# Kernel optimization log

Measured on AMD Instinct MI355X. Metric: run time of the kernel, lower is better.

## Reference

```python
import jax, jax.numpy as jnp
import numpy as np

N = 50000
E = 800000
IN = 128
H = 128
C = 64
BN_EPS = 1e-5


def gcn_conv(x, W, b, src, dst, n_nodes):
    # GCNConv: add self-loops, symmetric normalization D^-1/2 (A+I) D^-1/2, linear, bias
    deg = jax.ops.segment_sum(jnp.ones_like(dst, dtype=x.dtype), dst, num_segments=n_nodes)
    dinv = jnp.where(deg > 0, jax.lax.rsqrt(deg), jnp.zeros_like(deg))
    norm = dinv[src] * dinv[dst]                      # [E+N]
    h = x @ W                                         # [N, out]
    agg = jax.ops.segment_sum(norm[:, None] * h[src], dst, num_segments=n_nodes)
    return agg + b


def batch_norm_eval(x, gamma, beta, mean, var):
    return gamma * (x - mean) * jax.lax.rsqrt(var + BN_EPS) + beta


def setup_inputs() -> dict:
    key = jax.random.key(0)
    ks = jax.random.split(key, 16)
    inp = {
        "x": jax.random.normal(ks[0], (N, IN), dtype=jnp.float32),
        "edge_index": jax.random.randint(ks[1], (2, E), 0, N, dtype=jnp.int64),
        "W1": jax.random.normal(ks[2], (IN, H), dtype=jnp.float32) / np.sqrt(IN),
        "b1": jnp.zeros((H,), dtype=jnp.float32),
        "g1": jnp.ones((H,), dtype=jnp.float32),
        "be1": jnp.zeros((H,), dtype=jnp.float32),
        "m1": jax.random.normal(ks[3], (H,), dtype=jnp.float32) * 0.1,
        "v1": jax.random.uniform(ks[4], (H,), dtype=jnp.float32, minval=0.5, maxval=1.5),
        "W2": jax.random.normal(ks[5], (H, H), dtype=jnp.float32) / np.sqrt(H),
        "b2": jnp.zeros((H,), dtype=jnp.float32),
        "g2": jnp.ones((H,), dtype=jnp.float32),
        "be2": jnp.zeros((H,), dtype=jnp.float32),
        "m2": jax.random.normal(ks[6], (H,), dtype=jnp.float32) * 0.1,
        "v2": jax.random.uniform(ks[7], (H,), dtype=jnp.float32, minval=0.5, maxval=1.5),
        "W3": jax.random.normal(ks[8], (H, C), dtype=jnp.float32) / np.sqrt(H),
        "b3": jnp.zeros((C,), dtype=jnp.float32),
    }
    return inp


def reference(x, edge_index, W1, b1, g1, be1, m1, v1, W2, b2, g2, be2, m2, v2, W3, b3):
    # add self loops once (shared across layers, GCNConv cached=True)
    loop = jnp.arange(N, dtype=edge_index.dtype)
    src = jnp.concatenate([edge_index[0], loop])
    dst = jnp.concatenate([edge_index[1], loop])

    h = gcn_conv(x, W1, b1, src, dst, N)
    h = jax.nn.relu(batch_norm_eval(h, g1, be1, m1, v1))  # eval mode: dropout is identity
    h = gcn_conv(h, W2, b2, src, dst, N)
    h = jax.nn.relu(batch_norm_eval(h, g2, be2, m2, v2))
    out = gcn_conv(h, W3, b3, src, dst, N)
    return out
```

## Files before the change

### kernel.cpp

```cpp
#include <hip/hip_runtime.h>


#define SCAN_CHUNK 1024
#define NCHUNK 256
#define BSHIFT 8
#define BWID 256
#define ECAP 8192

typedef __attribute__((ext_vector_type(8))) short bf16x8;
typedef __attribute__((ext_vector_type(4))) float f32x4;

__device__ __forceinline__ float blo(unsigned p) { return __uint_as_float(p << 16); }
__device__ __forceinline__ float bhi(unsigned p) { return __uint_as_float(p & 0xffff0000u); }
__device__ __forceinline__ unsigned short f2b(float f) {
  unsigned u = __float_as_uint(f);
  unsigned r = (u + 0x7fffu + ((u >> 16) & 1u)) >> 16;
  return (unsigned short)r;
}

__global__ __launch_bounds__(256) void histprep_kernel(
    const int* __restrict__ ei32, const long long* __restrict__ ei64,
    int* __restrict__ counts, int E, int nbk,
    const float* __restrict__ W1, const float* __restrict__ W2,
    const float* __restrict__ W3,
    const float* __restrict__ b1, const float* __restrict__ g1,
    const float* __restrict__ be1, const float* __restrict__ m1,
    const float* __restrict__ v1,
    const float* __restrict__ b2, const float* __restrict__ g2,
    const float* __restrict__ be2, const float* __restrict__ m2,
    const float* __restrict__ v2,
    unsigned short* __restrict__ Wt1, unsigned short* __restrict__ Wt2,
    unsigned short* __restrict__ Wt3,
    float* __restrict__ sc1, float* __restrict__ sh1,
    float* __restrict__ sc2, float* __restrict__ sh2) {
  __shared__ int hist[BWID];
  __shared__ int s_is32;
  int k = blockIdx.x, t = threadIdx.x;
  if (k >= NCHUNK) {
    int i = (k - NCHUNK) * 256 + t;
    if (i < 16384) {
      int kk = i >> 7, c = i & 127;
      Wt1[c * 128 + kk] = f2b(W1[i]);
    } else if (i < 32768) {
      int j = i - 16384; int kk = j >> 7, c = j & 127;
      Wt2[c * 128 + kk] = f2b(W2[j]);
    } else if (i < 40960) {
      int j = i - 32768; int kk = j >> 6, c = j & 63;
      Wt3[c * 128 + kk] = f2b(W3[j]);
    } else if (i < 41088) {
      int c = i - 40960;
      float s = g1[c] * rsqrtf(v1[c] + 1e-5f);
      sc1[c] = s; sh1[c] = (b1[c] - m1[c]) * s + be1[c];
    } else if (i < 41216) {
      int c = i - 41088;
      float s = g2[c] * rsqrtf(v2[c] + 1e-5f);
      sc2[c] = s; sh2[c] = (b2[c] - m2[c]) * s + be2[c];
    }
    return;
  }
  hist[t] = 0;
  if (t == 0) s_is32 = 0;
  int CH = (E + NCHUNK - 1) / NCHUNK;
  int e0 = k * CH, e1 = min(e0 + CH, E);
  __syncthreads();
  if (t < 64 && e0 + t < E && ei32[2 * (e0 + t) + 1] != 0) atomicOr(&s_is32, 1);
  __syncthreads();
  int is32 = s_is32;
  for (int e = e0 + t; e < e1; e += 256) {
    int d = is32 ? ei32[E + e] : (int)ei64[E + e];
    atomicAdd(&hist[d >> BSHIFT], 1);
  }
  __syncthreads();
  if (t < nbk) counts[t * NCHUNK + k] = hist[t];
}

__global__ __launch_bounds__(256) void scan_partial_kernel(
    const int* __restrict__ src, int* __restrict__ bsum, int n) {
  __shared__ int wsum[4];
  int b = blockIdx.x, t = threadIdx.x;
  int lane = t & 63, wv = t >> 6;
  int i0 = b * SCAN_CHUNK + t * 4;
  int4 d4 = make_int4(0, 0, 0, 0);
  if (i0 + 3 < n) d4 = *(const int4*)&src[i0];
  else {
    if (i0 < n) d4.x = src[i0];
    if (i0 + 1 < n) d4.y = src[i0 + 1];
    if (i0 + 2 < n) d4.z = src[i0 + 2];
  }
  int s = d4.x + d4.y + d4.z + d4.w;
#pragma unroll
  for (int off = 32; off; off >>= 1) s += __shfl_xor(s, off);
  if (lane == 0) wsum[wv] = s;
  __syncthreads();
  if (t == 0) bsum[b] = wsum[0] + wsum[1] + wsum[2] + wsum[3];
}

__global__ __launch_bounds__(256) void scan_write_kernel(
    const int* __restrict__ src, const int* __restrict__ bsum,
    int* __restrict__ outp, int n, int nb) {
  __shared__ int woff[4];
  __shared__ int s_boff;
  int b = blockIdx.x, t = threadIdx.x;
  int lane = t & 63, wv = t >> 6;
  if (t < 64) {
    int v = (t < nb) ? bsum[t] : 0;
    int ic = v;
#pragma unroll
    for (int off = 1; off < 64; off <<= 1) {
      int u = __shfl_up(ic, off);
      if (t >= off) ic += u;
    }
    if (t == b) s_boff = ic - v;
    if (b == nb - 1 && t == 63) outp[n] = ic;
  }
  int i0 = b * SCAN_CHUNK + t * 4;
  int4 d4 = make_int4(0, 0, 0, 0);
  if (i0 + 3 < n) d4 = *(const int4*)&src[i0];
  else {
    if (i0 < n) d4.x = src[i0];
    if (i0 + 1 < n) d4.y = src[i0 + 1];
    if (i0 + 2 < n) d4.z = src[i0 + 2];
  }
  int tsum = d4.x + d4.y + d4.z + d4.w;
  int inc = tsum;
#pragma unroll
  for (int off = 1; off < 64; off <<= 1) {
    int u = __shfl_up(inc, off);
    if (lane >= off) inc += u;
  }
  if (lane == 63) woff[wv] = inc;
  __syncthreads();
  if (t == 0) {
    int r = 0;
#pragma unroll
    for (int w = 0; w < 4; ++w) { int sw = woff[w]; woff[w] = r; r += sw; }
  }
  __syncthreads();
  int p = inc - tsum + woff[wv] + s_boff;
  int dg[4] = {d4.x, d4.y, d4.z, d4.w};
#pragma unroll
  for (int j = 0; j < 4; ++j) {
    int i = i0 + j;
    if (i < n) outp[i] = p;
    p += dg[j];
  }
}

__global__ __launch_bounds__(256) void bin_scatter_kernel(
    const int* __restrict__ ei32, const long long* __restrict__ ei64,
    const int* __restrict__ offs, unsigned* __restrict__ pairs, int E, int nbk) {
  __shared__ int cur[BWID];
  __shared__ int s_is32;
  int k = blockIdx.x, t = threadIdx.x;
  if (t < nbk) cur[t] = offs[t * NCHUNK + k];
  if (t == 0) s_is32 = 0;
  int CH = (E + NCHUNK - 1) / NCHUNK;
  int e0 = k * CH, e1 = min(e0 + CH, E);
  __syncthreads();
  if (t < 64 && e0 + t < E && ei32[2 * (e0 + t) + 1] != 0) atomicOr(&s_is32, 1);
  __syncthreads();
  int is32 = s_is32;
  for (int e = e0 + t; e < e1; e += 256) {
    int s, d;
    if (is32) { s = ei32[e]; d = ei32[E + e]; }
    else      { s = (int)ei64[e]; d = (int)ei64[E + e]; }
    int pos = atomicAdd(&cur[d >> BSHIFT], 1);
    pairs[pos] = (unsigned)s | ((unsigned)(d & (BWID - 1)) << 20);
  }
}

__global__ __launch_bounds__(256) void bucket_merged_kernel(
    const unsigned* __restrict__ pairs, const int* __restrict__ offs,
    int* __restrict__ rowptr, float* __restrict__ dinv,
    int* __restrict__ col, int E, int n, int nbk) {
  __shared__ int deg[BWID];
  __shared__ int cur[BWID];
  __shared__ int woff[4];
  __shared__ int stage_s[ECAP];
  int b = blockIdx.x, t = threadIdx.x;
  int lane = t & 63, wv = t >> 6;
  deg[t] = 0;
  __syncthreads();
  int basep = offs[b * NCHUNK];
  int endp = (b + 1 < nbk) ? offs[(b + 1) * NCHUNK] : E;
  for (int i = basep + t; i < endp; i += 256)
    atomicAdd(&deg[pairs[i] >> 20], 1);
  __syncthreads();
  int dg = deg[t];
  int inc = dg;
#pragma unroll
  for (int off = 1; off < 64; off <<= 1) {
    int u = __shfl_up(inc, off);
    if (lane >= off) inc += u;
  }
  if (lane == 63) woff[wv] = inc;
  __syncthreads();
  if (t == 0) {
    int r = 0;
#pragma unroll
    for (int w = 0; w < 4; ++w) { int sw = woff[w]; woff[w] = r; r += sw; }
  }
  __syncthreads();
  int exc = inc - dg + woff[wv];
  int idx = b * BWID + t;
  if (idx < n) {
    rowptr[idx] = basep + exc;
    dinv[idx] = rsqrtf((float)(dg + 1));
  }
  cur[t] = exc;
  __syncthreads();
  for (int i = basep + t; i < endp; i += 256) {
    unsigned p = pairs[i];
    int s = (int)(p & 0xFFFFFu);
    int dl = (int)(p >> 20);
    int pos = atomicAdd(&cur[dl], 1);
    if (pos < ECAP) stage_s[pos] = s;
    else col[basep + pos] = s;
  }
  __syncthreads();
  int nE = endp - basep;
  int lim = min(nE, ECAP);
  for (int i = t; i < lim; i += 256) col[basep + i] = stage_s[i];
  if (b == 0 && t == 0) rowptr[n] = E;
}

template <int HOUT, int ABF16>
__global__ __launch_bounds__(256) void mgemm_kernel(
    const void* __restrict__ Ain, const unsigned short* __restrict__ Wt,
    unsigned short* __restrict__ Y, int n) {
  constexpr int NT = HOUT;
  __shared__ unsigned char AsB[64 * 256];
  __shared__ unsigned char BsB[NT * 256];
  int t = threadIdx.x;
  int row0 = blockIdx.x * 64;

  if constexpr (ABF16) {
    const unsigned short* A = (const unsigned short*)Ain;
#pragma unroll
    for (int jj = 0; jj < 4; ++jj) {
      int f = t + 256 * jj; int r = f >> 4, kq = f & 15;
      uint4 v = make_uint4(0, 0, 0, 0);
      if (row0 + r < n) v = *(const uint4*)&A[(size_t)(row0 + r) * 128 + kq * 8];
      *(uint4*)&AsB[r * 256 + ((kq * 16) ^ ((r & 15) << 4))] = v;
    }
  } else {
    const float* A = (const float*)Ain;
#pragma unroll
    for (int jj = 0; jj < 8; ++jj) {
      int f = t + 256 * jj; int r = f >> 5, kq = f & 31;
      float4 v = make_float4(0.f, 0.f, 0.f, 0.f);
      if (row0 + r < n) v = *(const float4*)&A[(size_t)(row0 + r) * 128 + kq * 4];
      unsigned two0 = (unsigned)f2b(v.x) | ((unsigned)f2b(v.y) << 16);
      unsigned two1 = (unsigned)f2b(v.z) | ((unsigned)f2b(v.w) << 16);
      uint2 o = make_uint2(two0, two1);
      *(uint2*)&AsB[r * 256 + ((kq * 8) ^ ((r & 15) << 4))] = o;
    }
  }
#pragma unroll
  for (int jj = 0; jj < NT / 16; ++jj) {
    int f = t + 256 * jj; int c = f >> 4, kq = f & 15;
    uint4 v = *(const uint4*)&Wt[(size_t)c * 128 + kq * 8];
    *(uint4*)&BsB[c * 256 + ((kq * 16) ^ ((c & 15) << 4))] = v;
  }
  __syncthreads();

  int l = t & 63, wid = t >> 6;
  constexpr int WC = NT / 2;
  constexpr int NI = WC / 16;
  int wr = (wid >> 1) * 32, wc = (wid & 1) * WC;
  int lr = l & 15, lk = (l >> 4) * 16;

  f32x4 acc[2][NI] = {};
#pragma unroll
  for (int ks = 0; ks < 4; ++ks) {
    bf16x8 a[2], b[NI];
#pragma unroll
    for (int mi = 0; mi < 2; ++mi) {
      int r = wr + mi * 16 + lr;
      a[mi] = *(const bf16x8*)&AsB[r * 256 + ((ks * 64 + lk) ^ ((r & 15) << 4))];
    }
#pragma unroll
    for (int ni = 0; ni < NI; ++ni) {
      int c = wc + ni * 16 + lr;
      b[ni] = *(const bf16x8*)&BsB[c * 256 + ((ks * 64 + lk) ^ ((c & 15) << 4))];
    }
#pragma unroll
    for (int mi = 0; mi < 2; ++mi)
#pragma unroll
      for (int ni = 0; ni < NI; ++ni)
        acc[mi][ni] = __builtin_amdgcn_mfma_f32_16x16x32_bf16(a[mi], b[ni],
                                                              acc[mi][ni], 0, 0, 0);
  }

#pragma unroll
  for (int mi = 0; mi < 2; ++mi) {
#pragma unroll
    for (int reg = 0; reg < 4; ++reg) {
      int gr = row0 + wr + mi * 16 + (l >> 4) * 4 + reg;
      if (gr < n) {
#pragma unroll
        for (int ni = 0; ni < NI; ++ni) {
          int gc = wc + ni * 16 + lr;
          Y[(size_t)gr * HOUT + gc] = f2b(acc[mi][ni][reg]);
        }
      }
    }
  }
}

template <int HOUT, bool BN, bool OUTBF>
__global__ __launch_bounds__(256) void agg_kernel(
    const unsigned short* __restrict__ h, const int* __restrict__ rowptr,
    const int* __restrict__ col, const float* __restrict__ dinv,
    const float* __restrict__ sc, const float* __restrict__ sh,
    void* __restrict__ out, int n_nodes) {
  int n = (blockIdx.x * blockDim.x + threadIdx.x) >> 6;
  if (n >= n_nodes) return;
  int lane = threadIdx.x & 63;
  const uint2* hu2 = (const uint2*)h;
  constexpr int RW2 = HOUT / 4;
  constexpr int NPH = (HOUT == 128) ? 2 : 4;
  constexpr int GL = 64 / NPH;
  int phase = lane / GL;
  int sub = lane & (GL - 1);

  float dn = dinv[n];
  int beg = rowptr[n], end = rowptr[n + 1];
  float a0 = 0.f, a1 = 0.f, a2 = 0.f, a3 = 0.f;
  if (phase == 0) {
    uint2 sp = hu2[(size_t)n * RW2 + sub];
    float sw = dn * dn;
    a0 = sw * blo(sp.x); a1 = sw * bhi(sp.x);
    a2 = sw * blo(sp.y); a3 = sw * bhi(sp.y);
  }

  int j = beg + phase;
  for (; j + 3 * NPH < end; j += 4 * NPH) {
    int s0 = col[j],           s1 = col[j + NPH];
    int s2 = col[j + 2 * NPH], s3 = col[j + 3 * NPH];
    uint2 h0 = hu2[(size_t)s0 * RW2 + sub];
    uint2 h1 = hu2[(size_t)s1 * RW2 + sub];
    uint2 h2 = hu2[(size_t)s2 * RW2 + sub];
    uint2 h3 = hu2[(size_t)s3 * RW2 + sub];
    float w0 = dn * dinv[s0], w1 = dn * dinv[s1];
    float w2 = dn * dinv[s2], w3 = dn * dinv[s3];
    a0 = fmaf(w0, blo(h0.x), a0); a1 = fmaf(w0, bhi(h0.x), a1);
    a2 = fmaf(w0, blo(h0.y), a2); a3 = fmaf(w0, bhi(h0.y), a3);
    a0 = fmaf(w1, blo(h1.x), a0); a1 = fmaf(w1, bhi(h1.x), a1);
    a2 = fmaf(w1, blo(h1.y), a2); a3 = fmaf(w1, bhi(h1.y), a3);
    a0 = fmaf(w2, blo(h2.x), a0); a1 = fmaf(w2, bhi(h2.x), a1);
    a2 = fmaf(w2, blo(h2.y), a2); a3 = fmaf(w2, bhi(h2.y), a3);
    a0 = fmaf(w3, blo(h3.x), a0); a1 = fmaf(w3, bhi(h3.x), a1);
    a2 = fmaf(w3, blo(h3.y), a2); a3 = fmaf(w3, bhi(h3.y), a3);
  }
  for (; j < end; j += NPH) {
    int s = col[j];
    uint2 hv = hu2[(size_t)s * RW2 + sub];
    float w = dn * dinv[s];
    a0 = fmaf(w, blo(hv.x), a0); a1 = fmaf(w, bhi(hv.x), a1);
    a2 = fmaf(w, blo(hv.y), a2); a3 = fmaf(w, bhi(hv.y), a3);
  }

  a0 += __shfl_xor(a0, 32); a1 += __shfl_xor(a1, 32);
  a2 += __shfl_xor(a2, 32); a3 += __shfl_xor(a3, 32);
  if constexpr (NPH == 4) {
    a0 += __shfl_xor(a0, 16); a1 += __shfl_xor(a1, 16);
    a2 += __shfl_xor(a2, 16); a3 += __shfl_xor(a3, 16);
  }
  if (phase != 0) return;

  int c0 = sub * 4;
  float y0, y1, y2, y3;
  if constexpr (BN) {
    y0 = fmaxf(fmaf(a0, sc[c0], sh[c0]), 0.f);
    y1 = fmaxf(fmaf(a1, sc[c0 + 1], sh[c0 + 1]), 0.f);
    y2 = fmaxf(fmaf(a2, sc[c0 + 2], sh[c0 + 2]), 0.f);
    y3 = fmaxf(fmaf(a3, sc[c0 + 3], sh[c0 + 3]), 0.f);
  } else {
    y0 = a0 + sh[c0]; y1 = a1 + sh[c0 + 1];
    y2 = a2 + sh[c0 + 2]; y3 = a3 + sh[c0 + 3];
  }
  if constexpr (OUTBF) {
    unsigned p0 = (unsigned)f2b(y0) | ((unsigned)f2b(y1) << 16);
    unsigned p1 = (unsigned)f2b(y2) | ((unsigned)f2b(y3) << 16);
    ((uint2*)out)[(size_t)n * RW2 + sub] = make_uint2(p0, p1);
  } else {
    float4 o; o.x = y0; o.y = y1; o.z = y2; o.w = y3;
    *(float4*)&((float*)out)[(size_t)n * HOUT + c0] = o;
  }
}

extern "C" void kernel_launch(void* const* d_in, const int* in_sizes, int n_in,
                              void* d_out, int out_size, void* d_ws, size_t ws_size,
                              hipStream_t stream) {
  const float* x = (const float*)d_in[0];
  const int* ei32 = (const int*)d_in[1];
  const long long* ei64 = (const long long*)d_in[1];
  const float* W1 = (const float*)d_in[2];
  const float* b1 = (const float*)d_in[3];
  const float* g1 = (const float*)d_in[4];
  const float* be1 = (const float*)d_in[5];
  const float* m1 = (const float*)d_in[6];
  const float* v1 = (const float*)d_in[7];
  const float* W2 = (const float*)d_in[8];
  const float* b2 = (const float*)d_in[9];
  const float* g2 = (const float*)d_in[10];
  const float* be2 = (const float*)d_in[11];
  const float* m2 = (const float*)d_in[12];
  const float* v2 = (const float*)d_in[13];
  const float* W3 = (const float*)d_in[14];
  const float* b3 = (const float*)d_in[15];

  const int N = in_sizes[0] / 128;
  const int E = in_sizes[1] / 2;
  const int NBK = (N + BWID - 1) / BWID;
  const int NC = NBK * NCHUNK;

  char* ws = (char*)d_ws;
  size_t off = 0;
  auto alloc = [&](size_t bytes) -> void* {
    void* p = ws + off;
    off = (off + bytes + 255) & ~(size_t)255;
    return p;
  };
  float* dinv = (float*)alloc((size_t)N * 4);
  int* rowptr = (int*)alloc((size_t)(N + 1) * 4);
  int* counts = (int*)alloc((size_t)(NC + 1) * 4);
  int* offs = (int*)alloc((size_t)(NC + 1) * 4);
  int* col = (int*)alloc((size_t)E * 4);
  unsigned* pairs = (unsigned*)alloc((size_t)E * 4);
  int* bsum = (int*)alloc(64 * 4);
  unsigned short* wt1 = (unsigned short*)alloc(128 * 128 * 2);
  unsigned short* wt2 = (unsigned short*)alloc(128 * 128 * 2);
  unsigned short* wt3 = (unsigned short*)alloc(128 * 64 * 2);
  float* sc1 = (float*)alloc(128 * 4);
  float* sh1 = (float*)alloc(128 * 4);
  float* sc2 = (float*)alloc(128 * 4);
  float* sh2 = (float*)alloc(128 * 4);
  unsigned short* hbuf = (unsigned short*)alloc((size_t)N * 128 * 2);
  unsigned short* ybuf = (unsigned short*)alloc((size_t)N * 128 * 2);
  (void)ws_size;

  histprep_kernel<<<NCHUNK + 161, 256, 0, stream>>>(
      ei32, ei64, counts, E, NBK,
      W1, W2, W3, b1, g1, be1, m1, v1, b2, g2, be2, m2, v2,
      wt1, wt2, wt3, sc1, sh1, sc2, sh2);
  int nbC = (NC + SCAN_CHUNK - 1) / SCAN_CHUNK;
  scan_partial_kernel<<<nbC, 256, 0, stream>>>(counts, bsum, NC);
  scan_write_kernel<<<nbC, 256, 0, stream>>>(counts, bsum, offs, NC, nbC);
  bin_scatter_kernel<<<NCHUNK, 256, 0, stream>>>(ei32, ei64, offs, pairs, E, NBK);
  bucket_merged_kernel<<<NBK, 256, 0, stream>>>(pairs, offs, rowptr, dinv,
                                                col, E, N, NBK);

  int gb = (N + 63) / 64;
  int ab = (N + 3) / 4;

  mgemm_kernel<128, 0><<<gb, 256, 0, stream>>>(x, wt1, hbuf, N);
  agg_kernel<128, true, true><<<ab, 256, 0, stream>>>(hbuf, rowptr, col, dinv,
                                                      sc1, sh1, ybuf, N);
  mgemm_kernel<128, 1><<<gb, 256, 0, stream>>>(ybuf, wt2, hbuf, N);
  agg_kernel<128, true, true><<<ab, 256, 0, stream>>>(hbuf, rowptr, col, dinv,
                                                      sc2, sh2, ybuf, N);
  mgemm_kernel<64, 1><<<gb, 256, 0, stream>>>(ybuf, wt3, hbuf, N);
  agg_kernel<64, false, false><<<ab, 256, 0, stream>>>(hbuf, rowptr, col, dinv,
                                                       nullptr, b3, d_out, N);
}
```

Measured before the change: 165.5 us.

## Fuse aggregation+BN+ReLU with the next layer's GEMM via shared-memory tile

Layers 1 and 2 now run as one kernel each: every block aggregates 64 node rows (one wave handles 16 rows in turn), applies BN and ReLU, writes the bf16 result into a swizzled LDS tile, and multiplies it by the next weight matrix with MFMA. This removes the round trip of the intermediate activation through global memory and two kernel launches. The cost is that each wave now processes rows one after another, which exposes gather latency, and there are fewer blocks than the old one-node-per-wave aggregation had. The final aggregation stays separate, specialised to 64 channels.

```diff
diff --git a/kernel.cpp b/kernel.cpp
--- a/kernel.cpp
+++ b/kernel.cpp
@@ -224,9 +224,9 @@
   if (b == 0 && t == 0) rowptr[n] = E;
 }
 
-template <int HOUT, int ABF16>
+template <int HOUT>
 __global__ __launch_bounds__(256) void mgemm_kernel(
-    const void* __restrict__ Ain, const unsigned short* __restrict__ Wt,
+    const float* __restrict__ A, const unsigned short* __restrict__ Wt,
     unsigned short* __restrict__ Y, int n) {
   constexpr int NT = HOUT;
   __shared__ unsigned char AsB[64 * 256];
@@ -234,27 +234,15 @@
   int t = threadIdx.x;
   int row0 = blockIdx.x * 64;
 
-  if constexpr (ABF16) {
-    const unsigned short* A = (const unsigned short*)Ain;
-#pragma unroll
-    for (int jj = 0; jj < 4; ++jj) {
-      int f = t + 256 * jj; int r = f >> 4, kq = f & 15;
-      uint4 v = make_uint4(0, 0, 0, 0);
-      if (row0 + r < n) v = *(const uint4*)&A[(size_t)(row0 + r) * 128 + kq * 8];
-      *(uint4*)&AsB[r * 256 + ((kq * 16) ^ ((r & 15) << 4))] = v;
-    }
-  } else {
-    const float* A = (const float*)Ain;
-#pragma unroll
-    for (int jj = 0; jj < 8; ++jj) {
-      int f = t + 256 * jj; int r = f >> 5, kq = f & 31;
-      float4 v = make_float4(0.f, 0.f, 0.f, 0.f);
-      if (row0 + r < n) v = *(const float4*)&A[(size_t)(row0 + r) * 128 + kq * 4];
-      unsigned two0 = (unsigned)f2b(v.x) | ((unsigned)f2b(v.y) << 16);
-      unsigned two1 = (unsigned)f2b(v.z) | ((unsigned)f2b(v.w) << 16);
-      uint2 o = make_uint2(two0, two1);
-      *(uint2*)&AsB[r * 256 + ((kq * 8) ^ ((r & 15) << 4))] = o;
-    }
+#pragma unroll
+  for (int jj = 0; jj < 8; ++jj) {
+    int f = t + 256 * jj; int r = f >> 5, kq = f & 31;
+    float4 v = make_float4(0.f, 0.f, 0.f, 0.f);
+    if (row0 + r < n) v = *(const float4*)&A[(size_t)(row0 + r) * 128 + kq * 4];
+    unsigned two0 = (unsigned)f2b(v.x) | ((unsigned)f2b(v.y) << 16);
+    unsigned two1 = (unsigned)f2b(v.z) | ((unsigned)f2b(v.w) << 16);
+    uint2 o = make_uint2(two0, two1);
+    *(uint2*)&AsB[r * 256 + ((kq * 8) ^ ((r & 15) << 4))] = o;
   }
 #pragma unroll
   for (int jj = 0; jj < NT / 16; ++jj) {
@@ -308,40 +296,158 @@
   }
 }
 
-template <int HOUT, bool BN, bool OUTBF>
-__global__ __launch_bounds__(256) void agg_kernel(
+template <int NTOUT>
+__global__ __launch_bounds__(256) void aggmm_kernel(
     const unsigned short* __restrict__ h, const int* __restrict__ rowptr,
     const int* __restrict__ col, const float* __restrict__ dinv,
     const float* __restrict__ sc, const float* __restrict__ sh,
-    void* __restrict__ out, int n_nodes) {
+    const unsigned short* __restrict__ Wt, unsigned short* __restrict__ Y,
+    int n_nodes) {
+  __shared__ unsigned char ytile[64 * 256];
+  __shared__ unsigned char BsB[NTOUT * 256];
+  const uint2* hu2 = (const uint2*)h;
+  int t = threadIdx.x;
+  int wv = t >> 6, lane = t & 63;
+  int row0 = blockIdx.x * 64;
+
+#pragma unroll
+  for (int jj = 0; jj < NTOUT / 16; ++jj) {
+    int f = t + 256 * jj; int c = f >> 4, kq = f & 15;
+    uint4 v = *(const uint4*)&Wt[(size_t)c * 128 + kq * 8];
+    *(uint4*)&BsB[c * 256 + ((kq * 16) ^ ((c & 15) << 4))] = v;
+  }
+
+  int phase = lane >> 5;
+  int sub = lane & 31;
+
+  for (int i = 0; i < 16; ++i) {
+    int r = wv * 16 + i;
+    int n = row0 + r;
+    float a0 = 0.f, a1 = 0.f, a2 = 0.f, a3 = 0.f;
+    if (n < n_nodes) {
+      float dn = dinv[n];
+      int beg = rowptr[n], end = rowptr[n + 1];
+      if (phase == 0) {
+        uint2 sp = hu2[(size_t)n * 32 + sub];
+        float sw = dn * dn;
+        a0 = sw * blo(sp.x); a1 = sw * bhi(sp.x);
+        a2 = sw * blo(sp.y); a3 = sw * bhi(sp.y);
+      }
+      int j = beg + phase;
+      for (; j + 6 < end; j += 8) {
+        int s0 = col[j], s1 = col[j + 2], s2 = col[j + 4], s3 = col[j + 6];
+        uint2 h0 = hu2[(size_t)s0 * 32 + sub];
+        uint2 h1 = hu2[(size_t)s1 * 32 + sub];
+        uint2 h2 = hu2[(size_t)s2 * 32 + sub];
+        uint2 h3 = hu2[(size_t)s3 * 32 + sub];
+        float w0 = dn * dinv[s0], w1 = dn * dinv[s1];
+        float w2 = dn * dinv[s2], w3 = dn * dinv[s3];
+        a0 = fmaf(w0, blo(h0.x), a0); a1 = fmaf(w0, bhi(h0.x), a1);
+        a2 = fmaf(w0, blo(h0.y), a2); a3 = fmaf(w0, bhi(h0.y), a3);
+        a0 = fmaf(w1, blo(h1.x), a0); a1 = fmaf(w1, bhi(h1.x), a1);
+        a2 = fmaf(w1, blo(h1.y), a2); a3 = fmaf(w1, bhi(h1.y), a3);
+        a0 = fmaf(w2, blo(h2.x), a0); a1 = fmaf(w2, bhi(h2.x), a1);
+        a2 = fmaf(w2, blo(h2.y), a2); a3 = fmaf(w2, bhi(h2.y), a3);
+        a0 = fmaf(w3, blo(h3.x), a0); a1 = fmaf(w3, bhi(h3.x), a1);
+        a2 = fmaf(w3, blo(h3.y), a2); a3 = fmaf(w3, bhi(h3.y), a3);
+      }
+      for (; j < end; j += 2) {
+        int s = col[j];
+        uint2 hv = hu2[(size_t)s * 32 + sub];
+        float w = dn * dinv[s];
+        a0 = fmaf(w, blo(hv.x), a0); a1 = fmaf(w, bhi(hv.x), a1);
+        a2 = fmaf(w, blo(hv.y), a2); a3 = fmaf(w, bhi(hv.y), a3);
+      }
+    }
+    a0 += __shfl_xor(a0, 32); a1 += __shfl_xor(a1, 32);
+    a2 += __shfl_xor(a2, 32); a3 += __shfl_xor(a3, 32);
+    if (phase == 0) {
+      unsigned p0 = 0, p1 = 0;
+      if (n < n_nodes) {
+        int c0 = sub * 4;
+        float y0 = fmaxf(fmaf(a0, sc[c0], sh[c0]), 0.f);
+        float y1 = fmaxf(fmaf(a1, sc[c0 + 1], sh[c0 + 1]), 0.f);
+        float y2 = fmaxf(fmaf(a2, sc[c0 + 2], sh[c0 + 2]), 0.f);
+        float y3 = fmaxf(fmaf(a3, sc[c0 + 3], sh[c0 + 3]), 0.f);
+        p0 = (unsigned)f2b(y0) | ((unsigned)f2b(y1) << 16);
+        p1 = (unsigned)f2b(y2) | ((unsigned)f2b(y3) << 16);
+      }
+      int byte = r * 256 + (((sub >> 1) * 16) ^ ((r & 15) << 4)) + ((sub & 1) * 8);
+      *(uint2*)&ytile[byte] = make_uint2(p0, p1);
+    }
+  }
+  __syncthreads();
+
+  constexpr int WC = NTOUT / 2;
+  constexpr int NI = WC / 16;
+  int wr = (wv >> 1) * 32, wc = (wv & 1) * WC;
+  int lr = lane & 15, lk = (lane >> 4) * 16;
+
+  f32x4 acc[2][NI] = {};
+#pragma unroll
+  for (int ks = 0; ks < 4; ++ks) {
+    bf16x8 a[2], b[NI];
+#pragma unroll
+    for (int mi = 0; mi < 2; ++mi) {
+      int r = wr + mi * 16 + lr;
+      a[mi] = *(const bf16x8*)&ytile[r * 256 + ((ks * 64 + lk) ^ ((r & 15) << 4))];
+    }
+#pragma unroll
+    for (int ni = 0; ni < NI; ++ni) {
+      int c = wc + ni * 16 + lr;
+      b[ni] = *(const bf16x8*)&BsB[c * 256 + ((ks * 64 + lk) ^ ((c & 15) << 4))];
+    }
+#pragma unroll
+    for (int mi = 0; mi < 2; ++mi)
+#pragma unroll
+      for (int ni = 0; ni < NI; ++ni)
+        acc[mi][ni] = __builtin_amdgcn_mfma_f32_16x16x32_bf16(a[mi], b[ni],
+                                                              acc[mi][ni], 0, 0, 0);
+  }
+
+#pragma unroll
+  for (int mi = 0; mi < 2; ++mi) {
+#pragma unroll
+    for (int reg = 0; reg < 4; ++reg) {
+      int gr = row0 + wr + mi * 16 + (lane >> 4) * 4 + reg;
+      if (gr < n_nodes) {
+#pragma unroll
+        for (int ni = 0; ni < NI; ++ni) {
+          int gc = wc + ni * 16 + lr;
+          Y[(size_t)gr * NTOUT + gc] = f2b(acc[mi][ni][reg]);
+        }
+      }
+    }
+  }
+}
+
+__global__ __launch_bounds__(256) void agg64_kernel(
+    const unsigned short* __restrict__ h, const int* __restrict__ rowptr,
+    const int* __restrict__ col, const float* __restrict__ dinv,
+    const float* __restrict__ bias, float* __restrict__ out, int n_nodes) {
   int n = (blockIdx.x * blockDim.x + threadIdx.x) >> 6;
   if (n >= n_nodes) return;
   int lane = threadIdx.x & 63;
   const uint2* hu2 = (const uint2*)h;
-  constexpr int RW2 = HOUT / 4;
-  constexpr int NPH = (HOUT == 128) ? 2 : 4;
-  constexpr int GL = 64 / NPH;
-  int phase = lane / GL;
-  int sub = lane & (GL - 1);
+  int phase = lane >> 4;
+  int sub = lane & 15;
 
   float dn = dinv[n];
   int beg = rowptr[n], end = rowptr[n + 1];
   float a0 = 0.f, a1 = 0.f, a2 = 0.f, a3 = 0.f;
   if (phase == 0) {
-    uint2 sp = hu2[(size_t)n * RW2 + sub];
+    uint2 sp = hu2[(size_t)n * 16 + sub];
     float sw = dn * dn;
     a0 = sw * blo(sp.x); a1 = sw * bhi(sp.x);
     a2 = sw * blo(sp.y); a3 = sw * bhi(sp.y);
   }
-
   int j = beg + phase;
-  for (; j + 3 * NPH < end; j += 4 * NPH) {
-    int s0 = col[j],           s1 = col[j + NPH];
-    int s2 = col[j + 2 * NPH], s3 = col[j + 3 * NPH];
-    uint2 h0 = hu2[(size_t)s0 * RW2 + sub];
-    uint2 h1 = hu2[(size_t)s1 * RW2 + sub];
-    uint2 h2 = hu2[(size_t)s2 * RW2 + sub];
-    uint2 h3 = hu2[(size_t)s3 * RW2 + sub];
+  for (; j + 12 < end; j += 16) {
+    int s0 = col[j], s1 = col[j + 4], s2 = col[j + 8], s3 = col[j + 12];
+    uint2 h0 = hu2[(size_t)s0 * 16 + sub];
+    uint2 h1 = hu2[(size_t)s1 * 16 + sub];
+    uint2 h2 = hu2[(size_t)s2 * 16 + sub];
+    uint2 h3 = hu2[(size_t)s3 * 16 + sub];
     float w0 = dn * dinv[s0], w1 = dn * dinv[s1];
     float w2 = dn * dinv[s2], w3 = dn * dinv[s3];
     a0 = fmaf(w0, blo(h0.x), a0); a1 = fmaf(w0, bhi(h0.x), a1);
@@ -353,41 +459,23 @@
     a0 = fmaf(w3, blo(h3.x), a0); a1 = fmaf(w3, bhi(h3.x), a1);
     a2 = fmaf(w3, blo(h3.y), a2); a3 = fmaf(w3, bhi(h3.y), a3);
   }
-  for (; j < end; j += NPH) {
+  for (; j < end; j += 4) {
     int s = col[j];
-    uint2 hv = hu2[(size_t)s * RW2 + sub];
+    uint2 hv = hu2[(size_t)s * 16 + sub];
     float w = dn * dinv[s];
     a0 = fmaf(w, blo(hv.x), a0); a1 = fmaf(w, bhi(hv.x), a1);
     a2 = fmaf(w, blo(hv.y), a2); a3 = fmaf(w, bhi(hv.y), a3);
   }
-
   a0 += __shfl_xor(a0, 32); a1 += __shfl_xor(a1, 32);
   a2 += __shfl_xor(a2, 32); a3 += __shfl_xor(a3, 32);
-  if constexpr (NPH == 4) {
-    a0 += __shfl_xor(a0, 16); a1 += __shfl_xor(a1, 16);
-    a2 += __shfl_xor(a2, 16); a3 += __shfl_xor(a3, 16);
-  }
+  a0 += __shfl_xor(a0, 16); a1 += __shfl_xor(a1, 16);
+  a2 += __shfl_xor(a2, 16); a3 += __shfl_xor(a3, 16);
   if (phase != 0) return;
-
   int c0 = sub * 4;
-  float y0, y1, y2, y3;
-  if constexpr (BN) {
-    y0 = fmaxf(fmaf(a0, sc[c0], sh[c0]), 0.f);
-    y1 = fmaxf(fmaf(a1, sc[c0 + 1], sh[c0 + 1]), 0.f);
-    y2 = fmaxf(fmaf(a2, sc[c0 + 2], sh[c0 + 2]), 0.f);
-    y3 = fmaxf(fmaf(a3, sc[c0 + 3], sh[c0 + 3]), 0.f);
-  } else {
-    y0 = a0 + sh[c0]; y1 = a1 + sh[c0 + 1];
-    y2 = a2 + sh[c0 + 2]; y3 = a3 + sh[c0 + 3];
-  }
-  if constexpr (OUTBF) {
-    unsigned p0 = (unsigned)f2b(y0) | ((unsigned)f2b(y1) << 16);
-    unsigned p1 = (unsigned)f2b(y2) | ((unsigned)f2b(y3) << 16);
-    ((uint2*)out)[(size_t)n * RW2 + sub] = make_uint2(p0, p1);
-  } else {
-    float4 o; o.x = y0; o.y = y1; o.z = y2; o.w = y3;
-    *(float4*)&((float*)out)[(size_t)n * HOUT + c0] = o;
-  }
+  float4 o;
+  o.x = a0 + bias[c0];     o.y = a1 + bias[c0 + 1];
+  o.z = a2 + bias[c0 + 2]; o.w = a3 + bias[c0 + 3];
+  *(float4*)&out[(size_t)n * 64 + c0] = o;
 }
 
 extern "C" void kernel_launch(void* const* d_in, const int* in_sizes, int n_in,
@@ -437,8 +525,9 @@
   float* sh1 = (float*)alloc(128 * 4);
   float* sc2 = (float*)alloc(128 * 4);
   float* sh2 = (float*)alloc(128 * 4);
-  unsigned short* hbuf = (unsigned short*)alloc((size_t)N * 128 * 2);
-  unsigned short* ybuf = (unsigned short*)alloc((size_t)N * 128 * 2);
+  unsigned short* hbufA = (unsigned short*)alloc((size_t)N * 128 * 2);
+  unsigned short* hbufB = (unsigned short*)alloc((size_t)N * 128 * 2);
+  unsigned short* hbufC = (unsigned short*)alloc((size_t)N * 64 * 2);
   (void)ws_size;
 
   histprep_kernel<<<NCHUNK + 161, 256, 0, stream>>>(
@@ -455,13 +544,11 @@
   int gb = (N + 63) / 64;
   int ab = (N + 3) / 4;
 
-  mgemm_kernel<128, 0><<<gb, 256, 0, stream>>>(x, wt1, hbuf, N);
-  agg_kernel<128, true, true><<<ab, 256, 0, stream>>>(hbuf, rowptr, col, dinv,
-                                                      sc1, sh1, ybuf, N);
-  mgemm_kernel<128, 1><<<gb, 256, 0, stream>>>(ybuf, wt2, hbuf, N);
-  agg_kernel<128, true, true><<<ab, 256, 0, stream>>>(hbuf, rowptr, col, dinv,
-                                                      sc2, sh2, ybuf, N);
-  mgemm_kernel<64, 1><<<gb, 256, 0, stream>>>(ybuf, wt3, hbuf, N);
-  agg_kernel<64, false, false><<<ab, 256, 0, stream>>>(hbuf, rowptr, col, dinv,
-                                                       nullptr, b3, d_out, N);
-}
+  mgemm_kernel<128><<<gb, 256, 0, stream>>>(x, wt1, hbufA, N);
+  aggmm_kernel<128><<<gb, 256, 0, stream>>>(hbufA, rowptr, col, dinv,
+                                            sc1, sh1, wt2, hbufB, N);
+  aggmm_kernel<64><<<gb, 256, 0, stream>>>(hbufB, rowptr, col, dinv,
+                                           sc2, sh2, wt3, hbufC, N);
+  agg64_kernel<<<ab, 256, 0, stream>>>(hbufC, rowptr, col, dinv, b3,
+                                       (float*)d_out, N);
+}
```

Result: slower. 237.6 us (+43.6%).
